# Optimization experiments

Measured on AMD Instinct MI355X. Metric: run time of the kernel, lower is better.

Reference implementation:

```python
import jax, jax.numpy as jnp
import numpy as np

D = 1024
H = 16
HD = D // H  # per-head dim = 64
LQ = 2048
LK = 2048


def setup_inputs() -> dict:
    key = jax.random.key(0)
    ks = jax.random.split(key, 6)
    scale = 1.0 / np.sqrt(D)
    return {
        "input_embeddings": jax.random.normal(ks[0], (LQ, D), dtype=jnp.float32),
        "history_hidden": jax.random.normal(ks[1], (LK, D), dtype=jnp.float32),
        "W_q": jax.random.normal(ks[2], (D, D), dtype=jnp.float32) * scale,
        "W_k": jax.random.normal(ks[3], (D, D), dtype=jnp.float32) * scale,
        "W_v": jax.random.normal(ks[4], (D, D), dtype=jnp.float32) * scale,
        "W_o": jax.random.normal(ks[5], (D, D), dtype=jnp.float32) * scale,
    }


def reference(input_embeddings, history_hidden, W_q, W_k, W_v, W_o):
    # nn.Linear(bias=False): y = x @ W.T ; weights are [out, in]
    q = (input_embeddings @ W_q.T).reshape(LQ, H, HD)  # [Lq, H, hd]
    k = (history_hidden @ W_k.T).reshape(LK, H, HD)    # [Lk, H, hd]
    v = (history_hidden @ W_v.T).reshape(LK, H, HD)    # [Lk, H, hd]
    # per-head scaled dot-product attention, batched over heads
    scores = jnp.einsum("qhd,khd->hqk", q, k) / np.sqrt(HD).astype(np.float32)
    attn = jax.nn.softmax(scores, axis=-1)             # [H, Lq, Lk]
    ctx = jnp.einsum("hqk,khd->qhd", attn, v).reshape(LQ, D)
    # dropout p=0.0 -> identity
    return ctx @ W_o.T
```

## Files before the change

### kernel.cpp

```cpp
#include <hip/hip_runtime.h>

typedef __bf16 bf16x8 __attribute__((ext_vector_type(8)));
typedef __bf16 bf16x4 __attribute__((ext_vector_type(4)));
typedef float f32x4 __attribute__((ext_vector_type(4)));
typedef float f32x16 __attribute__((ext_vector_type(16)));
typedef unsigned short u16x4 __attribute__((ext_vector_type(4)));
typedef unsigned short u16x8 __attribute__((ext_vector_type(8)));

#define LQS 2048
#define LKS 2048
#define DMODEL 1024
#define NH 16
#define HDIM 64
#define NSPLIT 4
#define NT 8

#if __has_builtin(__builtin_amdgcn_exp2f)
#define EXP2(x) __builtin_amdgcn_exp2f(x)
#else
#define EXP2(x) exp2f(x)
#endif

#if __has_builtin(__builtin_amdgcn_mfma_f32_32x32x8bf16_1k)
#define HAS_K8 1
#else
#define HAS_K8 0
#endif

__device__ __forceinline__ unsigned short f2bf(float f) {
  union { float f; unsigned int u; } v; v.f = f;
  unsigned int r = v.u + 0x7FFFu + ((v.u >> 16) & 1u);
  return (unsigned short)(r >> 16);
}

__device__ __forceinline__ unsigned int pk2(float a, float b) {
  __bf16 lo = (__bf16)a, hi = (__bf16)b;
  unsigned short ul = __builtin_bit_cast(unsigned short, lo);
  unsigned short uh = __builtin_bit_cast(unsigned short, hi);
  return (unsigned)ul | ((unsigned)uh << 16);
}

#define ASYNC_CP16(gp, lp)                                                     \
  __builtin_amdgcn_global_load_lds(                                            \
      (const __attribute__((address_space(1))) unsigned int*)(gp),             \
      (__attribute__((address_space(3))) unsigned int*)(lp), 16, 0, 0)

struct CvtDesc { const float* src; unsigned short* dst; float scl; unsigned int nchunk; };
struct CvtBatch { CvtDesc d[6]; };

__global__ __launch_bounds__(256)
void cvt_all_k(CvtBatch cb) {
  unsigned int c = blockIdx.x * 256 + threadIdx.x;
#pragma unroll
  for (int s = 0; s < 6; ++s) {
    if (c < cb.d[s].nchunk) {
      const float* src = cb.d[s].src + (size_t)c * 8;
      float4 a = *(const float4*)(src);
      float4 b = *(const float4*)(src + 4);
      const float scl = cb.d[s].scl;
      u16x8 r;
      r[0] = f2bf(a.x * scl); r[1] = f2bf(a.y * scl);
      r[2] = f2bf(a.z * scl); r[3] = f2bf(a.w * scl);
      r[4] = f2bf(b.x * scl); r[5] = f2bf(b.y * scl);
      r[6] = f2bf(b.z * scl); r[7] = f2bf(b.w * scl);
      *(u16x8*)(cb.d[s].dst + (size_t)c * 8) = r;
      return;
    }
    c -= cb.d[s].nchunk;
  }
}

struct GemmDesc { const unsigned short* A; const unsigned short* B; void* C; int ldc; int transC; };
struct GemmBatch3 { GemmDesc d[3]; };

template<int BM, int BN, bool F32OUT>
__global__ __launch_bounds__(256)
void gemm_bt(GemmBatch3 gb, int K) {
  constexpr int MFR = BM / 32;
  constexpr int NFR = BN / 32;
  const GemmDesc g = gb.d[blockIdx.z];
  __shared__ __align__(16) unsigned short sA[2][BM * 32];
  __shared__ __align__(16) unsigned short sB[2][BN * 32];
  const int tid = threadIdx.x;
  const int w = tid >> 6, l = tid & 63;
  const int wr = w >> 1, wc = w & 1;
  const int lr = l & 15, lk = (l >> 4) * 8;
  const unsigned short* Ab = g.A + (size_t)(blockIdx.y * BM) * K;
  const unsigned short* Bb = g.B + (size_t)(blockIdx.x * BN) * K;
  const int srow = w * 16 + (l >> 2);
  const int scol = (((l & 3) ^ (srow & 3)) * 8);

  auto stage = [&](int buf, int k0) {
#pragma unroll
    for (int ia = 0; ia < BM / 64; ++ia)
      ASYNC_CP16(Ab + (size_t)(ia * 64 + srow) * K + k0 + scol,
                 sA[buf] + ia * 2048 + w * 512);
#pragma unroll
    for (int ib = 0; ib < BN / 64; ++ib)
      ASYNC_CP16(Bb + (size_t)(ib * 64 + srow) * K + k0 + scol,
                 sB[buf] + ib * 2048 + w * 512);
  };

  f32x4 acc[MFR][NFR] = {};
  stage(0, 0);
  __syncthreads();
  int cur = 0;
  for (int k0 = 0; k0 < K; k0 += 32) {
    if (k0 + 32 < K) stage(cur ^ 1, k0 + 32);
    bf16x8 af[MFR], bfr[NFR];
#pragma unroll
    for (int m = 0; m < MFR; ++m) {
      const int Ar = wr * (BM / 2) + m * 16 + lr;
      af[m] = *(const bf16x8*)(sA[cur] + Ar * 32 + (((l >> 4) ^ (Ar & 3)) * 8));
    }
#pragma unroll
    for (int n = 0; n < NFR; ++n) {
      const int Br = wc * (BN / 2) + n * 16 + lr;
      bfr[n] = *(const bf16x8*)(sB[cur] + Br * 32 + (((l >> 4) ^ (Br & 3)) * 8));
    }
#pragma unroll
    for (int m = 0; m < MFR; ++m)
#pragma unroll
      for (int n = 0; n < NFR; ++n)
        acc[m][n] = __builtin_amdgcn_mfma_f32_16x16x32_bf16(af[m], bfr[n], acc[m][n], 0, 0, 0);
    __syncthreads();
    cur ^= 1;
  }
  const int r0 = blockIdx.y * BM + wr * (BM / 2) + (l >> 4) * 4;
  const int c0 = blockIdx.x * BN + wc * (BN / 2) + lr;
  if (g.transC) {
#pragma unroll
    for (int m = 0; m < MFR; ++m)
#pragma unroll
      for (int n = 0; n < NFR; ++n) {
        u16x4 v;
#pragma unroll
        for (int r = 0; r < 4; ++r) v[r] = f2bf(acc[m][n][r]);
        *(u16x4*)((unsigned short*)g.C + (size_t)(c0 + n * 16) * g.ldc + r0 + m * 16) = v;
      }
  } else {
#pragma unroll
    for (int m = 0; m < MFR; ++m)
#pragma unroll
      for (int n = 0; n < NFR; ++n)
#pragma unroll
        for (int r = 0; r < 4; ++r) {
          size_t idx = (size_t)(r0 + m * 16 + r) * g.ldc + c0 + n * 16;
          if (F32OUT) ((float*)g.C)[idx] = acc[m][n][r];
          else        ((unsigned short*)g.C)[idx] = f2bf(acc[m][n][r]);
        }
  }
}

__global__ __launch_bounds__(256)
void attn_k(const unsigned short* __restrict__ Q, const unsigned short* __restrict__ K,
            const unsigned short* __restrict__ Vt,
            __bf16* __restrict__ pacc, float* __restrict__ plsum) {
  __shared__ __align__(16) __bf16 sK[3][64 * 64];
  __shared__ __align__(16) __bf16 sV[3][64 * 64];
  const int b = blockIdx.x;
  const int xcd = b & 7, rr = b >> 3;
  const int qt = rr & 15, chi = rr >> 4;
  const int c = xcd + 8 * chi;
  const int h = c & 15, z = c >> 4;
  const int tid = threadIdx.x;
  const int w = tid >> 6, l = tid & 63;
  const int lq = l & 31;
  const int hi = l >> 5;
  const int qw0 = qt * 128 + w * 32;

  const int srow = l >> 3;
  const int scolb = (l & 7) * 16;

  bf16x8 qf[4];
#pragma unroll
  for (int t = 0; t < 4; ++t)
    qf[t] = *(const bf16x8*)(Q + (size_t)(qw0 + lq) * DMODEL + h * HDIM + t * 16 + hi * 8);

  f32x16 accO[2] = {};
#if HAS_K8
  f32x16 accsum = {};
  bf16x4 onesv;
#pragma unroll
  for (int j = 0; j < 4; ++j) onesv[j] = (__bf16)1.0f;
#else
  float lrun = 0.f;
#endif

  const int kt0 = z * (LKS / NSPLIT);

#define STAGE(B, KT)                                                           \
  do {                                                                         \
    _Pragma("unroll")                                                          \
    for (int i_ = 0; i_ < 2; ++i_) {                                           \
      const int row_ = (w * 2 + i_) * 8 + srow;                                \
      const int sc_ = scolb ^ ((row_ & 7) << 4);                               \
      ASYNC_CP16(K + (size_t)((KT) + row_) * DMODEL + h * HDIM + sc_ / 2,      \
                 (char*)(&sK[B][0]) + (w * 2 + i_) * 1024);                    \
      ASYNC_CP16(Vt + (size_t)(h * HDIM + row_) * LKS + (KT) + sc_ / 2,        \
                 (char*)(&sV[B][0]) + (w * 2 + i_) * 1024);                    \
    }                                                                          \
  } while (0)

  STAGE(0, kt0);
  STAGE(1, kt0 + 64);

#pragma unroll
  for (int t = 0; t < NT; ++t) {
    if (t >= 1) {
      __builtin_amdgcn_sched_barrier(0);
      __builtin_amdgcn_s_barrier();
    }
    if (t + 2 < NT) STAGE((t + 2) % 3, kt0 + (t + 2) * 64);
    if (t < NT - 2)       asm volatile("s_waitcnt vmcnt(8)" ::: "memory");
    else if (t == NT - 2) asm volatile("s_waitcnt vmcnt(4)" ::: "memory");
    else                  asm volatile("s_waitcnt vmcnt(0)" ::: "memory");
    __builtin_amdgcn_s_barrier();
    __builtin_amdgcn_sched_barrier(0);
    const int cur = t % 3;

    f32x16 sc[2] = {};
#pragma unroll
    for (int kb = 0; kb < 2; ++kb)
#pragma unroll
      for (int tt = 0; tt < 4; ++tt) {
        const int krow = kb * 32 + lq;
        const int cb = (tt * 32 + hi * 16) ^ ((krow & 7) << 4);
        bf16x8 kf = *(const bf16x8*)((const char*)(&sK[cur][0]) + krow * 128 + cb);
        sc[kb] = __builtin_amdgcn_mfma_f32_32x32x16_bf16(kf, qf[tt], sc[kb], 0, 0, 0);
      }
#pragma unroll
    for (int kb = 0; kb < 2; ++kb)
#pragma unroll
      for (int r = 0; r < 16; ++r)
        sc[kb][r] = EXP2(sc[kb][r]);
    unsigned int wd[2][8];
#pragma unroll
    for (int kb = 0; kb < 2; ++kb)
#pragma unroll
      for (int g = 0; g < 8; ++g)
        wd[kb][g] = pk2(sc[kb][2 * g], sc[kb][2 * g + 1]);

#if HAS_K8
    union W2 { unsigned int u[2]; bf16x4 v; };
#pragma unroll
    for (int g = 0; g < 8; ++g) {
      W2 a;
      a.u[0] = wd[g >> 2][2 * (g & 3)];
      a.u[1] = wd[g >> 2][2 * (g & 3) + 1];
#pragma unroll
      for (int db = 0; db < 2; ++db) {
        const int vrow = db * 32 + lq;
        const int cb = (16 * g + 8 * hi) ^ ((vrow & 7) << 4);
        bf16x4 bv = *(const bf16x4*)((const char*)(&sV[cur][0]) + vrow * 128 + cb);
        accO[db] = __builtin_amdgcn_mfma_f32_32x32x8bf16_1k(a.v, bv, accO[db], 0, 0, 0);
      }
      accsum = __builtin_amdgcn_mfma_f32_32x32x8bf16_1k(a.v, onesv, accsum, 0, 0, 0);
    }
#else
#pragma unroll
    for (int kb = 0; kb < 2; ++kb)
#pragma unroll
      for (int r = 0; r < 16; ++r) lrun += sc[kb][r];
    union PA { unsigned int u[4]; bf16x8 v; };
    PA pa[4];
#pragma unroll
    for (int ks = 0; ks < 4; ++ks) {
      const int kb = ks >> 1;
      const int g0 = (ks & 1) * 4;
      const unsigned int own0 = wd[kb][g0],     own1 = wd[kb][g0 + 1];
      const unsigned int oth0 = wd[kb][g0 + 2], oth1 = wd[kb][g0 + 3];
      const unsigned int off0 = hi ? own0 : oth0;
      const unsigned int off1 = hi ? own1 : oth1;
      const unsigned int rcv0 = (unsigned int)__shfl_xor((int)off0, 32);
      const unsigned int rcv1 = (unsigned int)__shfl_xor((int)off1, 32);
      pa[ks].u[0] = hi ? rcv0 : own0;
      pa[ks].u[1] = hi ? rcv1 : own1;
      pa[ks].u[2] = hi ? oth0 : rcv0;
      pa[ks].u[3] = hi ? oth1 : rcv1;
    }
#pragma unroll
    for (int db = 0; db < 2; ++db)
#pragma unroll
      for (int ks = 0; ks < 4; ++ks) {
        const int vrow = db * 32 + lq;
        const int cb = (ks * 32 + hi * 16) ^ ((vrow & 7) << 4);
        bf16x8 vf = *(const bf16x8*)((const char*)(&sV[cur][0]) + vrow * 128 + cb);
        accO[db] = __builtin_amdgcn_mfma_f32_32x32x16_bf16(pa[ks].v, vf, accO[db], 0, 0, 0);
      }
#endif
  }
#undef STAGE

#if HAS_K8
  if (lq == 0) {
#pragma unroll
    for (int r = 0; r < 16; ++r)
      plsum[((size_t)z * NH + h) * LQS + qw0 + (r & 3) + 8 * (r >> 2) + 4 * hi] = accsum[r];
  }
#else
  lrun += __shfl_xor(lrun, 32);
  if (hi == 0)
    plsum[((size_t)z * NH + h) * LQS + qw0 + lq] = lrun;
#endif
#pragma unroll
  for (int db = 0; db < 2; ++db)
#pragma unroll
    for (int r = 0; r < 16; ++r) {
      const int q = qw0 + (r & 3) + 8 * (r >> 2) + 4 * hi;
      pacc[(size_t)z * LQS * DMODEL + (size_t)q * DMODEL + h * HDIM + db * 32 + lq] =
          (__bf16)accO[db][r];
    }
}

__global__ __launch_bounds__(256)
void combine_k(const __bf16* pacc, const float* __restrict__ plsum, __bf16* ctx) {
  const size_t e = ((size_t)blockIdx.x * 256 + threadIdx.x) * 8;
  const int row = (int)(e >> 10), d0 = (int)(e & 1023), h = d0 >> 6;
  float lsum = 0.f;
  float acc[8] = {};
#pragma unroll
  for (int z = 0; z < NSPLIT; ++z) {
    lsum += plsum[((size_t)z * NH + h) * LQS + row];
    bf16x8 v = *(const bf16x8*)(pacc + (size_t)z * LQS * DMODEL + e);
#pragma unroll
    for (int j = 0; j < 8; ++j) acc[j] += (float)v[j];
  }
  float inv = 1.0f / lsum;
  bf16x8 r;
#pragma unroll
  for (int j = 0; j < 8; ++j) r[j] = (__bf16)(acc[j] * inv);
  *(bf16x8*)(ctx + e) = r;
}

extern "C" void kernel_launch(void* const* d_in, const int* in_sizes, int n_in,
                              void* d_out, int out_size, void* d_ws, size_t ws_size,
                              hipStream_t stream) {
  const float* x  = (const float*)d_in[0];
  const float* hh = (const float*)d_in[1];
  const float* wq = (const float*)d_in[2];
  const float* wk = (const float*)d_in[3];
  const float* wv = (const float*)d_in[4];
  const float* wo = (const float*)d_in[5];

  unsigned short* ws = (unsigned short*)d_ws;
  const size_t E2 = (size_t)LQS * DMODEL;
  const size_t E1 = (size_t)DMODEL * DMODEL;
  const size_t M = 1048576;
  unsigned short* xb  = ws;
  unsigned short* hb  = ws + 2 * M;
  unsigned short* wqb = ws + 4 * M;
  unsigned short* wkb = ws + 5 * M;
  unsigned short* wvb = ws + 6 * M;
  unsigned short* wob = ws + 8 * M;
  unsigned short* Qb  = ws + 9 * M;
  unsigned short* Kb  = ws + 11 * M;
  unsigned short* Vtb = ws + 13 * M;
  __bf16* pacc  = (__bf16*)ws;
  float*  plsum = (float*)(ws + 15 * M);
  unsigned short* cxb = ws;
  const float SCL = 0.125f * 1.4426950408889634f;

  CvtBatch cb;
  cb.d[0] = { x,  xb,  SCL, (unsigned)(E2 / 8) };
  cb.d[1] = { hh, hb,  1.f, (unsigned)(E2 / 8) };
  cb.d[2] = { wq, wqb, 1.f, (unsigned)(E1 / 8) };
  cb.d[3] = { wk, wkb, 1.f, (unsigned)(E1 / 8) };
  cb.d[4] = { wv, wvb, 1.f, (unsigned)(E1 / 8) };
  cb.d[5] = { wo, wob, 1.f, (unsigned)(E1 / 8) };
  cvt_all_k<<<dim3(4096), 256, 0, stream>>>(cb);

  GemmBatch3 qkv;
  qkv.d[0] = { xb, wqb, (void*)Qb,  DMODEL, 0 };
  qkv.d[1] = { hb, wkb, (void*)Kb,  DMODEL, 0 };
  qkv.d[2] = { hb, wvb, (void*)Vtb, LKS,    1 };
  gemm_bt<64, 128, false>
      <<<dim3(DMODEL / 128, LQS / 64, 3), 256, 0, stream>>>(qkv, DMODEL);

  attn_k<<<dim3(16 * NH * NSPLIT), 256, 0, stream>>>(Qb, Kb, Vtb, pacc, plsum);

  combine_k<<<dim3((unsigned)(E2 / 2048)), 256, 0, stream>>>(pacc, plsum, (__bf16*)cxb);

  GemmBatch3 fin = {};
  fin.d[0] = { cxb, wob, d_out, DMODEL, 0 };
  gemm_bt<64, 64, true>
      <<<dim3(DMODEL / 64, LQS / 64, 1), 256, 0, stream>>>(fin, DMODEL);
}
```

Before: 91.35 us.

## Fuse split-K combine into attention via last-block counter and use 128-key tiles

Removes the separate combine kernel. Each attention block bumps a per-(query tile, head) atomic counter after writing its partial output, and the last of the NSPLIT blocks reduces the partials and writes the normalized context. The counters are zeroed by an extra block in the conversion kernel. The K/V staging also moves from 64-key triple-buffered tiles with hand-tuned waitcnt to 128-key double-buffered tiles with plain __syncthreads. This cuts the launch count and loop overhead, but it may lose the finer-grained load/compute overlap and adds a serialized tail reduction in one block per group.

```diff
diff --git a/kernel.cpp b/kernel.cpp
--- a/kernel.cpp
+++ b/kernel.cpp
@@ -13,7 +13,8 @@
 #define NH 16
 #define HDIM 64
 #define NSPLIT 4
-#define NT 8
+#define KVB 128
+#define NT 4
 
 #if __has_builtin(__builtin_amdgcn_exp2f)
 #define EXP2(x) __builtin_amdgcn_exp2f(x)
@@ -49,7 +50,11 @@
 struct CvtBatch { CvtDesc d[6]; };
 
 __global__ __launch_bounds__(256)
-void cvt_all_k(CvtBatch cb) {
+void cvt_all_k(CvtBatch cb, int* __restrict__ cnt) {
+  if (blockIdx.x == 4096) {
+    if (threadIdx.x < 256) cnt[threadIdx.x] = 0;
+    return;
+  }
   unsigned int c = blockIdx.x * 256 + threadIdx.x;
 #pragma unroll
   for (int s = 0; s < 6; ++s) {
@@ -155,9 +160,10 @@
 __global__ __launch_bounds__(256)
 void attn_k(const unsigned short* __restrict__ Q, const unsigned short* __restrict__ K,
             const unsigned short* __restrict__ Vt,
-            __bf16* __restrict__ pacc, float* __restrict__ plsum) {
-  __shared__ __align__(16) __bf16 sK[3][64 * 64];
-  __shared__ __align__(16) __bf16 sV[3][64 * 64];
+            __bf16* pacc, float* plsum, int* __restrict__ cnt, __bf16* ctx) {
+  __shared__ __align__(16) __bf16 sK[2][KVB * 64];
+  __shared__ __align__(16) __bf16 sV[2][64 * KVB];
+  __shared__ int lastf;
   const int b = blockIdx.x;
   const int xcd = b & 7, rr = b >> 3;
   const int qt = rr & 15, chi = rr >> 4;
@@ -169,9 +175,6 @@
   const int hi = l >> 5;
   const int qw0 = qt * 128 + w * 32;
 
-  const int srow = l >> 3;
-  const int scolb = (l & 7) * 16;
-
   bf16x8 qf[4];
 #pragma unroll
   for (int t = 0; t < 4; ++t)
@@ -192,59 +195,51 @@
 #define STAGE(B, KT)                                                           \
   do {                                                                         \
     _Pragma("unroll")                                                          \
-    for (int i_ = 0; i_ < 2; ++i_) {                                           \
-      const int row_ = (w * 2 + i_) * 8 + srow;                                \
-      const int sc_ = scolb ^ ((row_ & 7) << 4);                               \
-      ASYNC_CP16(K + (size_t)((KT) + row_) * DMODEL + h * HDIM + sc_ / 2,      \
-                 (char*)(&sK[B][0]) + (w * 2 + i_) * 1024);                    \
-      ASYNC_CP16(Vt + (size_t)(h * HDIM + row_) * LKS + (KT) + sc_ / 2,        \
-                 (char*)(&sV[B][0]) + (w * 2 + i_) * 1024);                    \
+    for (int i_ = 0; i_ < 4; ++i_) {                                           \
+      const int krow_ = w * 32 + i_ * 8 + (l >> 3);                            \
+      const int ksc_ = ((l & 7) * 16) ^ ((krow_ & 7) << 4);                    \
+      ASYNC_CP16(K + (size_t)((KT) + krow_) * DMODEL + h * HDIM + ksc_ / 2,    \
+                 (char*)(&sK[B][0]) + w * 4096 + i_ * 1024);                   \
+      const int vrow_ = w * 16 + i_ * 4 + (l >> 4);                            \
+      const int vsc_ = ((l & 15) * 16) ^ ((vrow_ & 7) << 4);                   \
+      ASYNC_CP16(Vt + (size_t)(h * HDIM + vrow_) * LKS + (KT) + vsc_ / 2,      \
+                 (char*)(&sV[B][0]) + w * 4096 + i_ * 1024);                   \
     }                                                                          \
   } while (0)
 
   STAGE(0, kt0);
-  STAGE(1, kt0 + 64);
-
-#pragma unroll
+  __syncthreads();
+  int cur = 0;
+
   for (int t = 0; t < NT; ++t) {
-    if (t >= 1) {
-      __builtin_amdgcn_sched_barrier(0);
-      __builtin_amdgcn_s_barrier();
-    }
-    if (t + 2 < NT) STAGE((t + 2) % 3, kt0 + (t + 2) * 64);
-    if (t < NT - 2)       asm volatile("s_waitcnt vmcnt(8)" ::: "memory");
-    else if (t == NT - 2) asm volatile("s_waitcnt vmcnt(4)" ::: "memory");
-    else                  asm volatile("s_waitcnt vmcnt(0)" ::: "memory");
-    __builtin_amdgcn_s_barrier();
-    __builtin_amdgcn_sched_barrier(0);
-    const int cur = t % 3;
-
-    f32x16 sc[2] = {};
-#pragma unroll
-    for (int kb = 0; kb < 2; ++kb)
+    if (t + 1 < NT) STAGE(cur ^ 1, kt0 + (t + 1) * KVB);
+
+    f32x16 sc4[4] = {};
+#pragma unroll
+    for (int kb = 0; kb < 4; ++kb)
 #pragma unroll
       for (int tt = 0; tt < 4; ++tt) {
         const int krow = kb * 32 + lq;
         const int cb = (tt * 32 + hi * 16) ^ ((krow & 7) << 4);
         bf16x8 kf = *(const bf16x8*)((const char*)(&sK[cur][0]) + krow * 128 + cb);
-        sc[kb] = __builtin_amdgcn_mfma_f32_32x32x16_bf16(kf, qf[tt], sc[kb], 0, 0, 0);
-      }
-#pragma unroll
-    for (int kb = 0; kb < 2; ++kb)
+        sc4[kb] = __builtin_amdgcn_mfma_f32_32x32x16_bf16(kf, qf[tt], sc4[kb], 0, 0, 0);
+      }
+#pragma unroll
+    for (int kb = 0; kb < 4; ++kb)
 #pragma unroll
       for (int r = 0; r < 16; ++r)
-        sc[kb][r] = EXP2(sc[kb][r]);
-    unsigned int wd[2][8];
-#pragma unroll
-    for (int kb = 0; kb < 2; ++kb)
+        sc4[kb][r] = EXP2(sc4[kb][r]);
+    unsigned int wd[4][8];
+#pragma unroll
+    for (int kb = 0; kb < 4; ++kb)
 #pragma unroll
       for (int g = 0; g < 8; ++g)
-        wd[kb][g] = pk2(sc[kb][2 * g], sc[kb][2 * g + 1]);
+        wd[kb][g] = pk2(sc4[kb][2 * g], sc4[kb][2 * g + 1]);
 
 #if HAS_K8
     union W2 { unsigned int u[2]; bf16x4 v; };
 #pragma unroll
-    for (int g = 0; g < 8; ++g) {
+    for (int g = 0; g < 16; ++g) {
       W2 a;
       a.u[0] = wd[g >> 2][2 * (g & 3)];
       a.u[1] = wd[g >> 2][2 * (g & 3) + 1];
@@ -252,43 +247,43 @@
       for (int db = 0; db < 2; ++db) {
         const int vrow = db * 32 + lq;
         const int cb = (16 * g + 8 * hi) ^ ((vrow & 7) << 4);
-        bf16x4 bv = *(const bf16x4*)((const char*)(&sV[cur][0]) + vrow * 128 + cb);
+        bf16x4 bv = *(const bf16x4*)((const char*)(&sV[cur][0]) + vrow * 256 + cb);
         accO[db] = __builtin_amdgcn_mfma_f32_32x32x8bf16_1k(a.v, bv, accO[db], 0, 0, 0);
       }
       accsum = __builtin_amdgcn_mfma_f32_32x32x8bf16_1k(a.v, onesv, accsum, 0, 0, 0);
     }
 #else
 #pragma unroll
-    for (int kb = 0; kb < 2; ++kb)
-#pragma unroll
-      for (int r = 0; r < 16; ++r) lrun += sc[kb][r];
+    for (int kb = 0; kb < 4; ++kb)
+#pragma unroll
+      for (int r = 0; r < 16; ++r) lrun += sc4[kb][r];
     union PA { unsigned int u[4]; bf16x8 v; };
-    PA pa[4];
-#pragma unroll
-    for (int ks = 0; ks < 4; ++ks) {
+#pragma unroll
+    for (int ks = 0; ks < 8; ++ks) {
       const int kb = ks >> 1;
       const int g0 = (ks & 1) * 4;
+      PA pa;
       const unsigned int own0 = wd[kb][g0],     own1 = wd[kb][g0 + 1];
       const unsigned int oth0 = wd[kb][g0 + 2], oth1 = wd[kb][g0 + 3];
       const unsigned int off0 = hi ? own0 : oth0;
       const unsigned int off1 = hi ? own1 : oth1;
       const unsigned int rcv0 = (unsigned int)__shfl_xor((int)off0, 32);
       const unsigned int rcv1 = (unsigned int)__shfl_xor((int)off1, 32);
-      pa[ks].u[0] = hi ? rcv0 : own0;
-      pa[ks].u[1] = hi ? rcv1 : own1;
-      pa[ks].u[2] = hi ? oth0 : rcv0;
-      pa[ks].u[3] = hi ? oth1 : rcv1;
-    }
-#pragma unroll
-    for (int db = 0; db < 2; ++db)
-#pragma unroll
-      for (int ks = 0; ks < 4; ++ks) {
+      pa.u[0] = hi ? rcv0 : own0;
+      pa.u[1] = hi ? rcv1 : own1;
+      pa.u[2] = hi ? oth0 : rcv0;
+      pa.u[3] = hi ? oth1 : rcv1;
+#pragma unroll
+      for (int db = 0; db < 2; ++db) {
         const int vrow = db * 32 + lq;
         const int cb = (ks * 32 + hi * 16) ^ ((vrow & 7) << 4);
-        bf16x8 vf = *(const bf16x8*)((const char*)(&sV[cur][0]) + vrow * 128 + cb);
-        accO[db] = __builtin_amdgcn_mfma_f32_32x32x16_bf16(pa[ks].v, vf, accO[db], 0, 0, 0);
-      }
-#endif
+        bf16x8 vf = *(const bf16x8*)((const char*)(&sV[cur][0]) + vrow * 256 + cb);
+        accO[db] = __builtin_amdgcn_mfma_f32_32x32x16_bf16(pa.v, vf, accO[db], 0, 0, 0);
+      }
+    }
+#endif
+    __syncthreads();
+    cur ^= 1;
   }
 #undef STAGE
 
@@ -311,26 +306,38 @@
       pacc[(size_t)z * LQS * DMODEL + (size_t)q * DMODEL + h * HDIM + db * 32 + lq] =
           (__bf16)accO[db][r];
     }
-}
-
-__global__ __launch_bounds__(256)
-void combine_k(const __bf16* pacc, const float* __restrict__ plsum, __bf16* ctx) {
-  const size_t e = ((size_t)blockIdx.x * 256 + threadIdx.x) * 8;
-  const int row = (int)(e >> 10), d0 = (int)(e & 1023), h = d0 >> 6;
-  float lsum = 0.f;
-  float acc[8] = {};
-#pragma unroll
-  for (int z = 0; z < NSPLIT; ++z) {
-    lsum += plsum[((size_t)z * NH + h) * LQS + row];
-    bf16x8 v = *(const bf16x8*)(pacc + (size_t)z * LQS * DMODEL + e);
-#pragma unroll
-    for (int j = 0; j < 8; ++j) acc[j] += (float)v[j];
-  }
-  float inv = 1.0f / lsum;
-  bf16x8 r;
-#pragma unroll
-  for (int j = 0; j < 8; ++j) r[j] = (__bf16)(acc[j] * inv);
-  *(bf16x8*)(ctx + e) = r;
+
+  __threadfence();
+  if (tid == 0) {
+    int old = atomicAdd(&cnt[qt * NH + h], 1);
+    lastf = (old == NSPLIT - 1) ? 1 : 0;
+  }
+  __syncthreads();
+  if (lastf) {
+    __threadfence();
+    const int qbase = qt * 128;
+    for (int it = tid; it < 1024; it += 256) {
+      const int row = qbase + (it >> 3);
+      const int c8 = (it & 7) * 8;
+      float lsum = 0.f;
+#pragma unroll
+      for (int zz = 0; zz < NSPLIT; ++zz)
+        lsum += plsum[((size_t)zz * NH + h) * LQS + row];
+      const size_t off = (size_t)row * DMODEL + h * HDIM + c8;
+      float a8[8] = {};
+#pragma unroll
+      for (int zz = 0; zz < NSPLIT; ++zz) {
+        bf16x8 v = *(const bf16x8*)(pacc + (size_t)zz * LQS * DMODEL + off);
+#pragma unroll
+        for (int j = 0; j < 8; ++j) a8[j] += (float)v[j];
+      }
+      const float inv = 1.0f / lsum;
+      u16x8 o;
+#pragma unroll
+      for (int j = 0; j < 8; ++j) o[j] = f2bf(a8[j] * inv);
+      *(u16x8*)((unsigned short*)ctx + off) = o;
+    }
+  }
 }
 
 extern "C" void kernel_launch(void* const* d_in, const int* in_sizes, int n_in,
@@ -358,6 +365,7 @@
   unsigned short* Vtb = ws + 13 * M;
   __bf16* pacc  = (__bf16*)ws;
   float*  plsum = (float*)(ws + 15 * M);
+  int*    cnt   = (int*)(ws + 15 * M + 262144);
   unsigned short* cxb = ws;
   const float SCL = 0.125f * 1.4426950408889634f;
 
@@ -368,7 +376,7 @@
   cb.d[3] = { wk, wkb, 1.f, (unsigned)(E1 / 8) };
   cb.d[4] = { wv, wvb, 1.f, (unsigned)(E1 / 8) };
   cb.d[5] = { wo, wob, 1.f, (unsigned)(E1 / 8) };
-  cvt_all_k<<<dim3(4096), 256, 0, stream>>>(cb);
+  cvt_all_k<<<dim3(4097), 256, 0, stream>>>(cb, cnt);
 
   GemmBatch3 qkv;
   qkv.d[0] = { xb, wqb, (void*)Qb,  DMODEL, 0 };
@@ -377,9 +385,8 @@
   gemm_bt<64, 128, false>
       <<<dim3(DMODEL / 128, LQS / 64, 3), 256, 0, stream>>>(qkv, DMODEL);
 
-  attn_k<<<dim3(16 * NH * NSPLIT), 256, 0, stream>>>(Qb, Kb, Vtb, pacc, plsum);
-
-  combine_k<<<dim3((unsigned)(E2 / 2048)), 256, 0, stream>>>(pacc, plsum, (__bf16*)cxb);
+  attn_k<<<dim3(16 * NH * NSPLIT), 256, 0, stream>>>(Qb, Kb, Vtb, pacc, plsum,
+                                                     cnt, (__bf16*)cxb);
 
   GemmBatch3 fin = {};
   fin.d[0] = { cxb, wob, d_out, DMODEL, 0 };
```

Result: slower. 220.3 us (+141.2%).
